# Performance work log

Hardware: AMD Instinct MI355X
Metric: run time of the kernel (lower is better)

Reference implementation:

```python
import jax, jax.numpy as jnp
import numpy as np

B, P = 16, 1024
D_TIME, NUM_MODS = 8, 22
DIM_S = NUM_MODS + D_TIME + 1  # 31
PHI_W, N_HEADS, DP = 32, 4, 32
PSI_W, PSI_L, RHO_W = 64, 64, 64
SQRT_DP = float(np.sqrt(DP))


def setup_inputs() -> dict:
    key = jax.random.key(0)
    ks = jax.random.split(key, 16)
    rn = lambda k, shape: jax.random.normal(k, shape, jnp.float32) * 0.05
    return dict(
        times=jax.random.uniform(ks[0], (B, P), jnp.float32) * 48.0,
        values=jax.random.normal(ks[1], (B, P), jnp.float32),
        measurements=jax.random.randint(ks[2], (B, P), 0, NUM_MODS + 1),
        non_pad_mask=jnp.ones((B, P, 1), jnp.float32),
        W_psi1=rn(ks[3], (DIM_S, PSI_W)), b_psi1=jnp.zeros((PSI_W,), jnp.float32),
        W_psi2=rn(ks[4], (PSI_W, PSI_L)), b_psi2=jnp.zeros((PSI_L,), jnp.float32),
        W_key=rn(ks[5], (DIM_S + PSI_L, N_HEADS * DP)), b_key=jnp.zeros((N_HEADS * DP,), jnp.float32),
        query=rn(ks[6], (N_HEADS, DP)),
        W_phi1=rn(ks[7], (DIM_S, PHI_W)), b_phi1=jnp.zeros((PHI_W,), jnp.float32),
        W_phi2=rn(ks[8], (PHI_W, PHI_W)), b_phi2=jnp.zeros((PHI_W,), jnp.float32),
        W_rho1=rn(ks[9], (N_HEADS * PHI_W, RHO_W)), b_rho1=jnp.zeros((RHO_W,), jnp.float32),
        W_rho2=rn(ks[10], (RHO_W, RHO_W)), b_rho2=jnp.zeros((RHO_W,), jnp.float32),
    )


def _temporal_enc(times):
    i = np.arange(D_TIME)
    pos_vec = jnp.asarray(10000.0 ** (2.0 * (i // 2) / D_TIME), jnp.float32)
    ang = times[:, :, None] / pos_vec  # [B,P,d_time]
    return jnp.where(jnp.asarray(i % 2 == 0), jnp.sin(ang), jnp.cos(ang))


def reference(times, values, measurements, non_pad_mask,
              W_psi1, b_psi1, W_psi2, b_psi2, W_key, b_key, query,
              W_phi1, b_phi1, W_phi2, b_phi2, W_rho1, b_rho1, W_rho2, b_rho2):
    m = non_pad_mask  # [B,P,1]
    te = _temporal_enc(times)
    oh = jax.nn.one_hot(measurements, NUM_MODS + 1, dtype=jnp.float32)[:, :, 1:]
    x = jnp.concatenate([te, values[:, :, None], oh], axis=-1)  # [B,P,dim_s]

    # CumulativeSetAttentionLayer: psi MLP -> cumulative mean -> keys . query
    psi = jax.nn.relu(jax.nn.relu(x @ W_psi1 + b_psi1) @ W_psi2 + b_psi2)  # [B,P,psi_l]
    cum = jnp.cumsum(psi * m, axis=1) / jnp.cumsum(m, axis=1)
    keys = (jnp.concatenate([x, cum], axis=-1) @ W_key + b_key).reshape(B, P, N_HEADS, DP)
    pre = jnp.einsum('bpmd,md->bpm', keys, query) / SQRT_DP  # [B,P,m]

    # phi MLP
    phi = jax.nn.relu(jax.nn.relu(x @ W_phi1 + b_phi1) @ W_phi2 + b_phi2) * m  # [B,P,phi_w]

    # cumulative softmax weighting (online path)
    cmax = jax.lax.cummax(pre, axis=1)  # [B,P,m], running max for stability
    D = jnp.exp(pre[:, None, :, :] - cmax[:, :, None, :])  # [B,P,Q,m]
    causal = jnp.arange(P)[:, None] >= jnp.arange(P)[None, :]  # keep Q <= P
    D = D * causal[None, :, :, None]
    E = D.sum(axis=2)  # [B,P,m]
    agg = jnp.einsum('bpqm,bqd->bpmd', D, phi) / E[:, :, :, None]
    agg = (agg * m[:, :, :, None]).reshape(B, P, N_HEADS * PHI_W)

    # rho MLP (return_sequences)
    out = jax.nn.relu(jax.nn.relu(agg @ W_rho1 + b_rho1) @ W_rho2 + b_rho2) * m
    return out
```

## Files before the change

kernel.cpp:

```cpp
#include <hip/hip_runtime.h>
#include <hip/hip_bf16.h>

#define B_ 16
#define P_ 1024
#define T_ (B_*P_)
#define CH_ 32
#define CL_ (P_/CH_)

constexpr int OFF_A     = 16;
constexpr int OFF_WPSI1 = 400;
constexpr int OFF_BPSI1 = OFF_WPSI1 + 1984;
constexpr int OFF_WPSI2 = OFF_BPSI1 + 64;
constexpr int OFF_BPSI2 = OFF_WPSI2 + 4096;
constexpr int OFF_WPHI1 = OFF_BPSI2 + 64;
constexpr int OFF_BPHI1 = OFF_WPHI1 + 992;
constexpr int OFF_WPHI2 = OFF_BPHI1 + 32;
constexpr int OFF_BPHI2 = OFF_WPHI2 + 1024;
constexpr int OFF_WRHO1 = OFF_BPHI2 + 32;
constexpr int OFF_BRHO1 = OFF_WRHO1 + 8192;
constexpr int OFF_WRHO2 = OFF_BRHO1 + 64;
constexpr int OFF_BRHO2 = OFF_WRHO2 + 4096;
constexpr int OFF_PHI   = OFF_BRHO2 + 64;
constexpr int OFF_Z     = OFF_PHI   + T_*32;
constexpr int OFF_PREX  = OFF_Z     + T_*4;
constexpr int OFF_EXPW  = OFF_PREX  + T_*4;
constexpr int OFF_CE    = OFF_EXPW  + T_*4;
constexpr int OFF_CS    = OFF_CE    + 2048;
constexpr int OFF_AGG   = OFF_CS    + 65536;

static __device__ __forceinline__ bool detect_f32(const void* mask_raw) {
  return ((*(const unsigned*)mask_raw) & 0xFFFFu) == 0u;
}
static __device__ __forceinline__ float ld_any(const void* src, int i, bool isf32) {
  if (isf32) return ((const float*)src)[i];
  return __bfloat162float(((const __hip_bfloat16*)src)[i]);
}

__global__ __launch_bounds__(256) void s01_prep(
    float* __restrict__ ws, const void* mask,
    const void* Wpsi1, const void* bpsi1, const void* Wpsi2, const void* bpsi2,
    const void* Wkey,  const void* bkey,  const void* query,
    const void* Wphi1, const void* bphi1, const void* Wphi2, const void* bphi2,
    const void* Wrho1, const void* brho1, const void* Wrho2, const void* brho2) {
  const bool isf32 = detect_f32(mask);
  if (blockIdx.x < 2) {
    const int gid = blockIdx.x * 256 + threadIdx.x;
    if (gid >= 384) return;
    const float inv_s = 0.17677669529663687f;
    const int h = gid & 3;
    const int j = gid >> 2;
    float s = 0.f;
    if (j < 95) {
      for (int d = 0; d < 32; ++d)
        s += ld_any(Wkey, j * 128 + h * 32 + d, isf32) * ld_any(query, h * 32 + d, isf32);
    } else {
      for (int d = 0; d < 32; ++d)
        s += ld_any(bkey, h * 32 + d, isf32) * ld_any(query, h * 32 + d, isf32);
    }
    ws[OFF_A + gid] = s * inv_s;
    return;
  }
  const int g  = (blockIdx.x - 2) * 256 + threadIdx.x;
  const int gs = (gridDim.x - 2) * 256;
  auto st = [&](int off, const void* src, int n) {
    for (int i = g; i < n; i += gs) ws[off + i] = ld_any(src, i, isf32);
  };
  st(OFF_WPSI1, Wpsi1, 1984); st(OFF_BPSI1, bpsi1, 64);
  st(OFF_WPSI2, Wpsi2, 4096); st(OFF_BPSI2, bpsi2, 64);
  st(OFF_WPHI1, Wphi1, 992);  st(OFF_BPHI1, bphi1, 32);
  st(OFF_WPHI2, Wphi2, 1024); st(OFF_BPHI2, bphi2, 32);
  st(OFF_WRHO1, Wrho1, 8192); st(OFF_BRHO1, brho1, 64);
  st(OFF_WRHO2, Wrho2, 4096); st(OFF_BRHO2, brho2, 64);
}

__global__ __launch_bounds__(256) void k1_token(float* __restrict__ ws,
                                                const int* __restrict__ measp,
                                                const void* __restrict__ times,
                                                const void* __restrict__ values,
                                                const void* __restrict__ mask) {
  __shared__ float sh1[4][64];
  __shared__ float sg1[4][32];
  const bool isf32 = detect_f32(mask);
  const int tid = threadIdx.x;
  const int wv  = __builtin_amdgcn_readfirstlane(tid >> 6);
  const int j   = tid & 63;
  const int t   = blockIdx.x * 4 + wv;

  const float tval = ld_any(times, t, isf32);
  const float vval = ld_any(values, t, isf32);
  const float mval = ld_any(mask, t, isf32);
  const int   meas = measp[t];
  const float sel  = (meas > 0) ? 1.f : 0.f;
  const int   mrow = (meas > 0) ? (8 + meas) : 0;

  float x[9];
  const float posv[4] = {1.f, 10.f, 100.f, 1000.f};
  #pragma unroll
  for (int k = 0; k < 4; ++k) {
    float s, c;
    __sincosf(tval / posv[k], &s, &c);
    x[2*k] = s; x[2*k+1] = c;
  }
  x[8] = vval;

  float h1 = ws[OFF_BPSI1 + j];
  #pragma unroll
  for (int i = 0; i < 9; ++i) h1 = fmaf(x[i], ws[OFF_WPSI1 + i * 64 + j], h1);
  h1 = fmaf(sel, ws[OFF_WPSI1 + mrow * 64 + j], h1);
  sh1[wv][j] = fmaxf(h1, 0.f);

  if (j < 32) {
    float g1 = ws[OFF_BPHI1 + j];
    #pragma unroll
    for (int i = 0; i < 9; ++i) g1 = fmaf(x[i], ws[OFF_WPHI1 + i * 32 + j], g1);
    g1 = fmaf(sel, ws[OFF_WPHI1 + mrow * 32 + j], g1);
    sg1[wv][j] = fmaxf(g1, 0.f);
  }
  __syncthreads();

  float h2 = ws[OFF_BPSI2 + j];
  #pragma unroll 8
  for (int i = 0; i < 64; ++i) h2 = fmaf(sh1[wv][i], ws[OFF_WPSI2 + i * 64 + j], h2);
  const float q = fmaxf(h2, 0.f) * mval;

  const float* a2 = ws + OFF_A + (31 + j) * 4;
  float z0 = q * a2[0], z1 = q * a2[1], z2 = q * a2[2], z3 = q * a2[3];
  #pragma unroll
  for (int off = 32; off; off >>= 1) {
    z0 += __shfl_xor(z0, off, 64);
    z1 += __shfl_xor(z1, off, 64);
    z2 += __shfl_xor(z2, off, 64);
    z3 += __shfl_xor(z3, off, 64);
  }
  if (j == 0) {
    float* zo = ws + OFF_Z + (size_t)t * 4;
    zo[0] = z0; zo[1] = z1; zo[2] = z2; zo[3] = z3;
  }

  if (j < 32) {
    float g2 = ws[OFF_BPHI2 + j];
    #pragma unroll 8
    for (int i = 0; i < 32; ++i) g2 = fmaf(sg1[wv][i], ws[OFF_WPHI2 + i * 32 + j], g2);
    ws[OFF_PHI + (size_t)t * 32 + j] = fmaxf(g2, 0.f) * mval;
  } else if (j < 36) {
    const int h = j - 32;
    float pr = ws[OFF_A + 380 + h];
    #pragma unroll
    for (int i = 0; i < 9; ++i) pr = fmaf(x[i], ws[OFF_A + i * 4 + h], pr);
    pr = fmaf(sel, ws[OFF_A + mrow * 4 + h], pr);
    ws[OFF_PREX + (size_t)t * 4 + h] = pr;
  }
}

__global__ __launch_bounds__(256) void k2_scanz(float* __restrict__ ws,
                                                const void* __restrict__ mask) {
  const int b   = blockIdx.x;
  const int tid = threadIdx.x;
  const bool isf32 = detect_f32(mask);
  __shared__ float sc[256], s0[256], s1[256], s2[256], s3[256];

  const float* zB = ws + OFF_Z + (size_t)b * P_ * 4;
  const int p0 = tid * 4;

  float lc[4], l0[4], l1[4], l2[4], l3[4];
  float c = 0.f, z0 = 0.f, z1 = 0.f, z2 = 0.f, z3 = 0.f;
  #pragma unroll
  for (int i = 0; i < 4; ++i) {
    c  += ld_any(mask, b * P_ + p0 + i, isf32);
    z0 += zB[(p0 + i) * 4 + 0]; z1 += zB[(p0 + i) * 4 + 1];
    z2 += zB[(p0 + i) * 4 + 2]; z3 += zB[(p0 + i) * 4 + 3];
    lc[i] = c; l0[i] = z0; l1[i] = z1; l2[i] = z2; l3[i] = z3;
  }

  float rc = c, r0 = z0, r1 = z1, r2 = z2, r3 = z3;
  sc[tid] = rc; s0[tid] = r0; s1[tid] = r1; s2[tid] = r2; s3[tid] = r3;
  __syncthreads();
  for (int off = 1; off < 256; off <<= 1) {
    float ac = 0.f, a0 = 0.f, a1 = 0.f, a2 = 0.f, a3 = 0.f;
    if (tid >= off) {
      ac = sc[tid - off]; a0 = s0[tid - off]; a1 = s1[tid - off];
      a2 = s2[tid - off]; a3 = s3[tid - off];
    }
    __syncthreads();
    rc += ac; r0 += a0; r1 += a1; r2 += a2; r3 += a3;
    sc[tid] = rc; s0[tid] = r0; s1[tid] = r1; s2[tid] = r2; s3[tid] = r3;
    __syncthreads();
  }
  const float ec = rc - c, e0 = r0 - z0, e1 = r1 - z1, e2 = r2 - z2, e3 = r3 - z3;

  const float* px = ws + OFF_PREX + (size_t)b * P_ * 4;
  float pre[4][4];
  float mx0 = -1e30f, mx1 = -1e30f, mx2 = -1e30f, mx3 = -1e30f;
  #pragma unroll
  for (int i = 0; i < 4; ++i) {
    const float inv = 1.f / (ec + lc[i]);
    const int p = p0 + i;
    pre[i][0] = px[p * 4 + 0] + (e0 + l0[i]) * inv;
    pre[i][1] = px[p * 4 + 1] + (e1 + l1[i]) * inv;
    pre[i][2] = px[p * 4 + 2] + (e2 + l2[i]) * inv;
    pre[i][3] = px[p * 4 + 3] + (e3 + l3[i]) * inv;
    mx0 = fmaxf(mx0, pre[i][0]); mx1 = fmaxf(mx1, pre[i][1]);
    mx2 = fmaxf(mx2, pre[i][2]); mx3 = fmaxf(mx3, pre[i][3]);
  }

  __syncthreads();
  s0[tid] = mx0; s1[tid] = mx1; s2[tid] = mx2; s3[tid] = mx3;
  __syncthreads();
  for (int off = 128; off; off >>= 1) {
    if (tid < off) {
      s0[tid] = fmaxf(s0[tid], s0[tid + off]);
      s1[tid] = fmaxf(s1[tid], s1[tid + off]);
      s2[tid] = fmaxf(s2[tid], s2[tid + off]);
      s3[tid] = fmaxf(s3[tid], s3[tid + off]);
    }
    __syncthreads();
  }
  const float M0 = s0[0], M1 = s1[0], M2 = s2[0], M3 = s3[0];

  float* eB = ws + OFF_EXPW + (size_t)b * P_ * 4;
  #pragma unroll
  for (int i = 0; i < 4; ++i) {
    const int p = p0 + i;
    eB[p * 4 + 0] = __expf(pre[i][0] - M0);
    eB[p * 4 + 1] = __expf(pre[i][1] - M1);
    eB[p * 4 + 2] = __expf(pre[i][2] - M2);
    eB[p * 4 + 3] = __expf(pre[i][3] - M3);
  }
}

__global__ __launch_bounds__(128) void k4a_sums(float* __restrict__ ws) {
  const int ch = blockIdx.x, b = blockIdx.y;
  const int h = threadIdx.x >> 5, d = threadIdx.x & 31;
  const float* eB   = ws + OFF_EXPW + (size_t)b * P_ * 4;
  const float* phiB = ws + OFF_PHI  + (size_t)b * P_ * 32;

  float E = 0.f, S = 0.f;
  const int pbeg = ch * CL_;
  #pragma unroll 4
  for (int p = pbeg; p < pbeg + CL_; ++p) {
    const float e  = eB[p * 4 + h];
    const float ph = phiB[p * 32 + d];
    E += e;
    S = fmaf(e, ph, S);
  }
  const int base = (b * CH_ + ch) * 4 + h;
  if (d == 0) ws[OFF_CE + base] = E;
  ws[OFF_CS + base * 32 + d] = S;
}

__global__ __launch_bounds__(128) void k4c_replay(float* __restrict__ ws,
                                                  const void* __restrict__ mask) {
  const int ch = blockIdx.x, b = blockIdx.y;
  const int h = threadIdx.x >> 5, d = threadIdx.x & 31;
  const bool isf32 = detect_f32(mask);
  const float* eB   = ws + OFF_EXPW + (size_t)b * P_ * 4;
  const float* phiB = ws + OFF_PHI  + (size_t)b * P_ * 32;
  float*       aggB = ws + OFF_AGG  + (size_t)b * P_ * 128;

  float E = 0.f, S = 0.f;
  for (int c2 = 0; c2 < ch; ++c2) {
    const int base2 = (b * CH_ + c2) * 4 + h;
    E += ws[OFF_CE + base2];
    S += ws[OFF_CS + base2 * 32 + d];
  }

  const int pbeg = ch * CL_;
  for (int p = pbeg; p < pbeg + CL_; ++p) {
    const float e  = eB[p * 4 + h];
    const float ph = phiB[p * 32 + d];
    E += e;
    S = fmaf(e, ph, S);
    aggB[p * 128 + h * 32 + d] = (S / E) * ld_any(mask, b * P_ + p, isf32);
  }
}

__global__ __launch_bounds__(256) void k5_rho(const float* __restrict__ ws,
                                              const void* __restrict__ mask_raw,
                                              void* __restrict__ out) {
  __shared__ float sW1[128 * 64];
  __shared__ float sH1[16][64];
  const int tid = threadIdx.x;
  for (int i = tid; i < 128 * 64; i += 256) sW1[i] = ws[OFF_WRHO1 + i];

  const int wv = __builtin_amdgcn_readfirstlane(tid >> 6);
  const int j  = tid & 63;
  const int t0 = blockIdx.x * 16 + wv * 4;
  const float* aggB = ws + OFF_AGG;

  const float b1 = ws[OFF_BRHO1 + j];
  float a0 = b1, a1 = b1, a2 = b1, a3 = b1;
  __syncthreads();

  #pragma unroll 8
  for (int i = 0; i < 128; ++i) {
    const float w = sW1[i * 64 + j];
    a0 = fmaf(aggB[(size_t)(t0 + 0) * 128 + i], w, a0);
    a1 = fmaf(aggB[(size_t)(t0 + 1) * 128 + i], w, a1);
    a2 = fmaf(aggB[(size_t)(t0 + 2) * 128 + i], w, a2);
    a3 = fmaf(aggB[(size_t)(t0 + 3) * 128 + i], w, a3);
  }
  sH1[wv * 4 + 0][j] = fmaxf(a0, 0.f);
  sH1[wv * 4 + 1][j] = fmaxf(a1, 0.f);
  sH1[wv * 4 + 2][j] = fmaxf(a2, 0.f);
  sH1[wv * 4 + 3][j] = fmaxf(a3, 0.f);
  __syncthreads();

  const float b2 = ws[OFF_BRHO2 + j];
  float o0 = b2, o1 = b2, o2 = b2, o3 = b2;
  #pragma unroll 8
  for (int i = 0; i < 64; ++i) {
    const float w = ws[OFF_WRHO2 + i * 64 + j];
    o0 = fmaf(sH1[wv * 4 + 0][i], w, o0);
    o1 = fmaf(sH1[wv * 4 + 1][i], w, o1);
    o2 = fmaf(sH1[wv * 4 + 2][i], w, o2);
    o3 = fmaf(sH1[wv * 4 + 3][i], w, o3);
  }

  const bool isf32 = detect_f32(mask_raw);
  float r[4] = {o0, o1, o2, o3};
  #pragma unroll
  for (int k = 0; k < 4; ++k) {
    const int t = t0 + k;
    const float v = fmaxf(r[k], 0.f) * ld_any(mask_raw, t, isf32);
    if (isf32) {
      ((float*)out)[(size_t)t * 64 + j] = v;
    } else {
      ((__hip_bfloat16*)out)[(size_t)t * 64 + j] = __float2bfloat16(v);
    }
  }
}

extern "C" void kernel_launch(void* const* d_in, const int* in_sizes, int n_in,
                              void* d_out, int out_size, void* d_ws, size_t ws_size,
                              hipStream_t stream) {
  const int* meas = (const int*)d_in[2];
  const void* times = d_in[0];
  const void* values = d_in[1];
  const void* mask = d_in[3];
  float* ws = (float*)d_ws;

  s01_prep<<<34, 256, 0, stream>>>(ws, mask,
                                   d_in[4], d_in[5], d_in[6], d_in[7],
                                   d_in[8], d_in[9], d_in[10],
                                   d_in[11], d_in[12], d_in[13], d_in[14],
                                   d_in[15], d_in[16], d_in[17], d_in[18]);
  k1_token<<<T_/4, 256, 0, stream>>>(ws, meas, times, values, mask);
  k2_scanz<<<B_, 256, 0, stream>>>(ws, mask);
  k4a_sums<<<dim3(CH_, B_), 128, 0, stream>>>(ws);
  k4c_replay<<<dim3(CH_, B_), 128, 0, stream>>>(ws, mask);
  k5_rho<<<T_/16, 256, 0, stream>>>(ws, mask, d_out);
}
```

Before: 160.3 us.

## Fuse all stages into one cooperative persistent kernel with grid syncs

Replaces the six separate kernel launches with a single cooperative kernel of 512 blocks that runs the weight prep, token MLPs, per-batch scan, chunk sums, replay and rho MLP as phases separated by grid.sync(). Shared memory is unioned across phases, and the token and rho stages loop over multiple tiles per block. This removes launch overhead and inter-kernel gaps. In exchange it adds grid-wide barrier costs and leaves most blocks idle during the 16-block scan phase.

```diff
diff --git a/kernel.cpp b/kernel.cpp
--- a/kernel.cpp
+++ b/kernel.cpp
@@ -1,11 +1,14 @@
 #include <hip/hip_runtime.h>
 #include <hip/hip_bf16.h>
+#include <hip/hip_cooperative_groups.h>
+namespace cg = cooperative_groups;
 
 #define B_ 16
 #define P_ 1024
 #define T_ (B_*P_)
 #define CH_ 32
 #define CL_ (P_/CH_)
+#define NBLK_ 512
 
 constexpr int OFF_A     = 16;
 constexpr int OFF_WPSI1 = 400;
@@ -36,317 +39,317 @@
   return __bfloat162float(((const __hip_bfloat16*)src)[i]);
 }
 
-__global__ __launch_bounds__(256) void s01_prep(
-    float* __restrict__ ws, const void* mask,
+__global__ __launch_bounds__(256, 2) void mega(
+    float* __restrict__ ws, const int* __restrict__ measp,
+    const void* times, const void* values, const void* mask, void* out,
     const void* Wpsi1, const void* bpsi1, const void* Wpsi2, const void* bpsi2,
     const void* Wkey,  const void* bkey,  const void* query,
     const void* Wphi1, const void* bphi1, const void* Wphi2, const void* bphi2,
     const void* Wrho1, const void* brho1, const void* Wrho2, const void* brho2) {
-  const bool isf32 = detect_f32(mask);
-  if (blockIdx.x < 2) {
-    const int gid = blockIdx.x * 256 + threadIdx.x;
-    if (gid >= 384) return;
-    const float inv_s = 0.17677669529663687f;
-    const int h = gid & 3;
-    const int j = gid >> 2;
-    float s = 0.f;
-    if (j < 95) {
-      for (int d = 0; d < 32; ++d)
-        s += ld_any(Wkey, j * 128 + h * 32 + d, isf32) * ld_any(query, h * 32 + d, isf32);
-    } else {
-      for (int d = 0; d < 32; ++d)
-        s += ld_any(bkey, h * 32 + d, isf32) * ld_any(query, h * 32 + d, isf32);
-    }
-    ws[OFF_A + gid] = s * inv_s;
-    return;
-  }
-  const int g  = (blockIdx.x - 2) * 256 + threadIdx.x;
-  const int gs = (gridDim.x - 2) * 256;
-  auto st = [&](int off, const void* src, int n) {
-    for (int i = g; i < n; i += gs) ws[off + i] = ld_any(src, i, isf32);
-  };
-  st(OFF_WPSI1, Wpsi1, 1984); st(OFF_BPSI1, bpsi1, 64);
-  st(OFF_WPSI2, Wpsi2, 4096); st(OFF_BPSI2, bpsi2, 64);
-  st(OFF_WPHI1, Wphi1, 992);  st(OFF_BPHI1, bphi1, 32);
-  st(OFF_WPHI2, Wphi2, 1024); st(OFF_BPHI2, bphi2, 32);
-  st(OFF_WRHO1, Wrho1, 8192); st(OFF_BRHO1, brho1, 64);
-  st(OFF_WRHO2, Wrho2, 4096); st(OFF_BRHO2, brho2, 64);
-}
-
-__global__ __launch_bounds__(256) void k1_token(float* __restrict__ ws,
-                                                const int* __restrict__ measp,
-                                                const void* __restrict__ times,
-                                                const void* __restrict__ values,
-                                                const void* __restrict__ mask) {
-  __shared__ float sh1[4][64];
-  __shared__ float sg1[4][32];
-  const bool isf32 = detect_f32(mask);
-  const int tid = threadIdx.x;
-  const int wv  = __builtin_amdgcn_readfirstlane(tid >> 6);
-  const int j   = tid & 63;
-  const int t   = blockIdx.x * 4 + wv;
-
-  const float tval = ld_any(times, t, isf32);
-  const float vval = ld_any(values, t, isf32);
-  const float mval = ld_any(mask, t, isf32);
-  const int   meas = measp[t];
-  const float sel  = (meas > 0) ? 1.f : 0.f;
-  const int   mrow = (meas > 0) ? (8 + meas) : 0;
-
-  float x[9];
-  const float posv[4] = {1.f, 10.f, 100.f, 1000.f};
-  #pragma unroll
-  for (int k = 0; k < 4; ++k) {
-    float s, c;
-    __sincosf(tval / posv[k], &s, &c);
-    x[2*k] = s; x[2*k+1] = c;
-  }
-  x[8] = vval;
-
-  float h1 = ws[OFF_BPSI1 + j];
-  #pragma unroll
-  for (int i = 0; i < 9; ++i) h1 = fmaf(x[i], ws[OFF_WPSI1 + i * 64 + j], h1);
-  h1 = fmaf(sel, ws[OFF_WPSI1 + mrow * 64 + j], h1);
-  sh1[wv][j] = fmaxf(h1, 0.f);
-
-  if (j < 32) {
-    float g1 = ws[OFF_BPHI1 + j];
-    #pragma unroll
-    for (int i = 0; i < 9; ++i) g1 = fmaf(x[i], ws[OFF_WPHI1 + i * 32 + j], g1);
-    g1 = fmaf(sel, ws[OFF_WPHI1 + mrow * 32 + j], g1);
-    sg1[wv][j] = fmaxf(g1, 0.f);
-  }
-  __syncthreads();
-
-  float h2 = ws[OFF_BPSI2 + j];
-  #pragma unroll 8
-  for (int i = 0; i < 64; ++i) h2 = fmaf(sh1[wv][i], ws[OFF_WPSI2 + i * 64 + j], h2);
-  const float q = fmaxf(h2, 0.f) * mval;
-
-  const float* a2 = ws + OFF_A + (31 + j) * 4;
-  float z0 = q * a2[0], z1 = q * a2[1], z2 = q * a2[2], z3 = q * a2[3];
-  #pragma unroll
-  for (int off = 32; off; off >>= 1) {
-    z0 += __shfl_xor(z0, off, 64);
-    z1 += __shfl_xor(z1, off, 64);
-    z2 += __shfl_xor(z2, off, 64);
-    z3 += __shfl_xor(z3, off, 64);
-  }
-  if (j == 0) {
-    float* zo = ws + OFF_Z + (size_t)t * 4;
-    zo[0] = z0; zo[1] = z1; zo[2] = z2; zo[3] = z3;
-  }
-
-  if (j < 32) {
-    float g2 = ws[OFF_BPHI2 + j];
-    #pragma unroll 8
-    for (int i = 0; i < 32; ++i) g2 = fmaf(sg1[wv][i], ws[OFF_WPHI2 + i * 32 + j], g2);
-    ws[OFF_PHI + (size_t)t * 32 + j] = fmaxf(g2, 0.f) * mval;
-  } else if (j < 36) {
-    const int h = j - 32;
-    float pr = ws[OFF_A + 380 + h];
-    #pragma unroll
-    for (int i = 0; i < 9; ++i) pr = fmaf(x[i], ws[OFF_A + i * 4 + h], pr);
-    pr = fmaf(sel, ws[OFF_A + mrow * 4 + h], pr);
-    ws[OFF_PREX + (size_t)t * 4 + h] = pr;
-  }
-}
-
-__global__ __launch_bounds__(256) void k2_scanz(float* __restrict__ ws,
-                                                const void* __restrict__ mask) {
-  const int b   = blockIdx.x;
+  cg::grid_group grid = cg::this_grid();
+  __shared__ union {
+    struct { float h1[4][64]; float g1[4][32]; } p1;
+    struct { float sc[256], s0[256], s1[256], s2[256], s3[256]; } p2;
+    struct { float w1[8192]; float h1[16][64]; } p5;
+  } sm;
+
   const int tid = threadIdx.x;
   const bool isf32 = detect_f32(mask);
-  __shared__ float sc[256], s0[256], s1[256], s2[256], s3[256];
-
-  const float* zB = ws + OFF_Z + (size_t)b * P_ * 4;
-  const int p0 = tid * 4;
-
-  float lc[4], l0[4], l1[4], l2[4], l3[4];
-  float c = 0.f, z0 = 0.f, z1 = 0.f, z2 = 0.f, z3 = 0.f;
-  #pragma unroll
-  for (int i = 0; i < 4; ++i) {
-    c  += ld_any(mask, b * P_ + p0 + i, isf32);
-    z0 += zB[(p0 + i) * 4 + 0]; z1 += zB[(p0 + i) * 4 + 1];
-    z2 += zB[(p0 + i) * 4 + 2]; z3 += zB[(p0 + i) * 4 + 3];
-    lc[i] = c; l0[i] = z0; l1[i] = z1; l2[i] = z2; l3[i] = z3;
-  }
-
-  float rc = c, r0 = z0, r1 = z1, r2 = z2, r3 = z3;
-  sc[tid] = rc; s0[tid] = r0; s1[tid] = r1; s2[tid] = r2; s3[tid] = r3;
-  __syncthreads();
-  for (int off = 1; off < 256; off <<= 1) {
-    float ac = 0.f, a0 = 0.f, a1 = 0.f, a2 = 0.f, a3 = 0.f;
-    if (tid >= off) {
-      ac = sc[tid - off]; a0 = s0[tid - off]; a1 = s1[tid - off];
-      a2 = s2[tid - off]; a3 = s3[tid - off];
-    }
-    __syncthreads();
-    rc += ac; r0 += a0; r1 += a1; r2 += a2; r3 += a3;
-    sc[tid] = rc; s0[tid] = r0; s1[tid] = r1; s2[tid] = r2; s3[tid] = r3;
-    __syncthreads();
-  }
-  const float ec = rc - c, e0 = r0 - z0, e1 = r1 - z1, e2 = r2 - z2, e3 = r3 - z3;
-
-  const float* px = ws + OFF_PREX + (size_t)b * P_ * 4;
-  float pre[4][4];
-  float mx0 = -1e30f, mx1 = -1e30f, mx2 = -1e30f, mx3 = -1e30f;
-  #pragma unroll
-  for (int i = 0; i < 4; ++i) {
-    const float inv = 1.f / (ec + lc[i]);
-    const int p = p0 + i;
-    pre[i][0] = px[p * 4 + 0] + (e0 + l0[i]) * inv;
-    pre[i][1] = px[p * 4 + 1] + (e1 + l1[i]) * inv;
-    pre[i][2] = px[p * 4 + 2] + (e2 + l2[i]) * inv;
-    pre[i][3] = px[p * 4 + 3] + (e3 + l3[i]) * inv;
-    mx0 = fmaxf(mx0, pre[i][0]); mx1 = fmaxf(mx1, pre[i][1]);
-    mx2 = fmaxf(mx2, pre[i][2]); mx3 = fmaxf(mx3, pre[i][3]);
-  }
-
-  __syncthreads();
-  s0[tid] = mx0; s1[tid] = mx1; s2[tid] = mx2; s3[tid] = mx3;
-  __syncthreads();
-  for (int off = 128; off; off >>= 1) {
-    if (tid < off) {
-      s0[tid] = fmaxf(s0[tid], s0[tid + off]);
-      s1[tid] = fmaxf(s1[tid], s1[tid + off]);
-      s2[tid] = fmaxf(s2[tid], s2[tid + off]);
-      s3[tid] = fmaxf(s3[tid], s3[tid + off]);
-    }
-    __syncthreads();
-  }
-  const float M0 = s0[0], M1 = s1[0], M2 = s2[0], M3 = s3[0];
-
-  float* eB = ws + OFF_EXPW + (size_t)b * P_ * 4;
-  #pragma unroll
-  for (int i = 0; i < 4; ++i) {
-    const int p = p0 + i;
-    eB[p * 4 + 0] = __expf(pre[i][0] - M0);
-    eB[p * 4 + 1] = __expf(pre[i][1] - M1);
-    eB[p * 4 + 2] = __expf(pre[i][2] - M2);
-    eB[p * 4 + 3] = __expf(pre[i][3] - M3);
-  }
-}
-
-__global__ __launch_bounds__(128) void k4a_sums(float* __restrict__ ws) {
-  const int ch = blockIdx.x, b = blockIdx.y;
-  const int h = threadIdx.x >> 5, d = threadIdx.x & 31;
-  const float* eB   = ws + OFF_EXPW + (size_t)b * P_ * 4;
-  const float* phiB = ws + OFF_PHI  + (size_t)b * P_ * 32;
-
-  float E = 0.f, S = 0.f;
-  const int pbeg = ch * CL_;
-  #pragma unroll 4
-  for (int p = pbeg; p < pbeg + CL_; ++p) {
-    const float e  = eB[p * 4 + h];
-    const float ph = phiB[p * 32 + d];
-    E += e;
-    S = fmaf(e, ph, S);
-  }
-  const int base = (b * CH_ + ch) * 4 + h;
-  if (d == 0) ws[OFF_CE + base] = E;
-  ws[OFF_CS + base * 32 + d] = S;
-}
-
-__global__ __launch_bounds__(128) void k4c_replay(float* __restrict__ ws,
-                                                  const void* __restrict__ mask) {
-  const int ch = blockIdx.x, b = blockIdx.y;
-  const int h = threadIdx.x >> 5, d = threadIdx.x & 31;
-  const bool isf32 = detect_f32(mask);
-  const float* eB   = ws + OFF_EXPW + (size_t)b * P_ * 4;
-  const float* phiB = ws + OFF_PHI  + (size_t)b * P_ * 32;
-  float*       aggB = ws + OFF_AGG  + (size_t)b * P_ * 128;
-
-  float E = 0.f, S = 0.f;
-  for (int c2 = 0; c2 < ch; ++c2) {
-    const int base2 = (b * CH_ + c2) * 4 + h;
-    E += ws[OFF_CE + base2];
-    S += ws[OFF_CS + base2 * 32 + d];
-  }
-
-  const int pbeg = ch * CL_;
-  for (int p = pbeg; p < pbeg + CL_; ++p) {
-    const float e  = eB[p * 4 + h];
-    const float ph = phiB[p * 32 + d];
-    E += e;
-    S = fmaf(e, ph, S);
-    aggB[p * 128 + h * 32 + d] = (S / E) * ld_any(mask, b * P_ + p, isf32);
-  }
-}
-
-__global__ __launch_bounds__(256) void k5_rho(const float* __restrict__ ws,
-                                              const void* __restrict__ mask_raw,
-                                              void* __restrict__ out) {
-  __shared__ float sW1[128 * 64];
-  __shared__ float sH1[16][64];
-  const int tid = threadIdx.x;
-  for (int i = tid; i < 128 * 64; i += 256) sW1[i] = ws[OFF_WRHO1 + i];
-
   const int wv = __builtin_amdgcn_readfirstlane(tid >> 6);
   const int j  = tid & 63;
-  const int t0 = blockIdx.x * 16 + wv * 4;
+
+  {
+    const int g  = blockIdx.x * 256 + tid;
+    if (g < 384) {
+      const float inv_s = 0.17677669529663687f;
+      const int h = g & 3;
+      const int jj = g >> 2;
+      float s = 0.f;
+      if (jj < 95) {
+        for (int d = 0; d < 32; ++d)
+          s += ld_any(Wkey, jj * 128 + h * 32 + d, isf32) * ld_any(query, h * 32 + d, isf32);
+      } else {
+        for (int d = 0; d < 32; ++d)
+          s += ld_any(bkey, h * 32 + d, isf32) * ld_any(query, h * 32 + d, isf32);
+      }
+      ws[OFF_A + g] = s * inv_s;
+    }
+    const int gs = NBLK_ * 256;
+    auto st = [&](int off, const void* src, int n) {
+      for (int i = g; i < n; i += gs) ws[off + i] = ld_any(src, i, isf32);
+    };
+    st(OFF_WPSI1, Wpsi1, 1984); st(OFF_BPSI1, bpsi1, 64);
+    st(OFF_WPSI2, Wpsi2, 4096); st(OFF_BPSI2, bpsi2, 64);
+    st(OFF_WPHI1, Wphi1, 992);  st(OFF_BPHI1, bphi1, 32);
+    st(OFF_WPHI2, Wphi2, 1024); st(OFF_BPHI2, bphi2, 32);
+    st(OFF_WRHO1, Wrho1, 8192); st(OFF_BRHO1, brho1, 64);
+    st(OFF_WRHO2, Wrho2, 4096); st(OFF_BRHO2, brho2, 64);
+  }
+  grid.sync();
+
+  for (int it = 0; it < 8; ++it) {
+    const int t = it * (NBLK_ * 4) + blockIdx.x * 4 + wv;
+
+    const float tval = ld_any(times, t, isf32);
+    const float vval = ld_any(values, t, isf32);
+    const float mval = ld_any(mask, t, isf32);
+    const int   meas = measp[t];
+    const float sel  = (meas > 0) ? 1.f : 0.f;
+    const int   mrow = (meas > 0) ? (8 + meas) : 0;
+
+    float x[9];
+    const float posv[4] = {1.f, 10.f, 100.f, 1000.f};
+    #pragma unroll
+    for (int k = 0; k < 4; ++k) {
+      float s, c;
+      __sincosf(tval / posv[k], &s, &c);
+      x[2*k] = s; x[2*k+1] = c;
+    }
+    x[8] = vval;
+
+    float h1 = ws[OFF_BPSI1 + j];
+    #pragma unroll
+    for (int i = 0; i < 9; ++i) h1 = fmaf(x[i], ws[OFF_WPSI1 + i * 64 + j], h1);
+    h1 = fmaf(sel, ws[OFF_WPSI1 + mrow * 64 + j], h1);
+    sm.p1.h1[wv][j] = fmaxf(h1, 0.f);
+
+    if (j < 32) {
+      float g1 = ws[OFF_BPHI1 + j];
+      #pragma unroll
+      for (int i = 0; i < 9; ++i) g1 = fmaf(x[i], ws[OFF_WPHI1 + i * 32 + j], g1);
+      g1 = fmaf(sel, ws[OFF_WPHI1 + mrow * 32 + j], g1);
+      sm.p1.g1[wv][j] = fmaxf(g1, 0.f);
+    }
+    __syncthreads();
+
+    float h2 = ws[OFF_BPSI2 + j];
+    #pragma unroll 8
+    for (int i = 0; i < 64; ++i) h2 = fmaf(sm.p1.h1[wv][i], ws[OFF_WPSI2 + i * 64 + j], h2);
+    const float q = fmaxf(h2, 0.f) * mval;
+
+    const float* a2 = ws + OFF_A + (31 + j) * 4;
+    float z0 = q * a2[0], z1 = q * a2[1], z2 = q * a2[2], z3 = q * a2[3];
+    #pragma unroll
+    for (int off = 32; off; off >>= 1) {
+      z0 += __shfl_xor(z0, off, 64);
+      z1 += __shfl_xor(z1, off, 64);
+      z2 += __shfl_xor(z2, off, 64);
+      z3 += __shfl_xor(z3, off, 64);
+    }
+    if (j == 0) {
+      float* zo = ws + OFF_Z + (size_t)t * 4;
+      zo[0] = z0; zo[1] = z1; zo[2] = z2; zo[3] = z3;
+    }
+
+    if (j < 32) {
+      float g2 = ws[OFF_BPHI2 + j];
+      #pragma unroll 8
+      for (int i = 0; i < 32; ++i) g2 = fmaf(sm.p1.g1[wv][i], ws[OFF_WPHI2 + i * 32 + j], g2);
+      ws[OFF_PHI + (size_t)t * 32 + j] = fmaxf(g2, 0.f) * mval;
+    } else if (j < 36) {
+      const int h = j - 32;
+      float pr = ws[OFF_A + 380 + h];
+      #pragma unroll
+      for (int i = 0; i < 9; ++i) pr = fmaf(x[i], ws[OFF_A + i * 4 + h], pr);
+      pr = fmaf(sel, ws[OFF_A + mrow * 4 + h], pr);
+      ws[OFF_PREX + (size_t)t * 4 + h] = pr;
+    }
+    __syncthreads();
+  }
+  grid.sync();
+
+  if (blockIdx.x < B_) {
+    const int b = blockIdx.x;
+    float* sc = sm.p2.sc; float* s0 = sm.p2.s0; float* s1 = sm.p2.s1;
+    float* s2 = sm.p2.s2; float* s3 = sm.p2.s3;
+
+    const float* zB = ws + OFF_Z + (size_t)b * P_ * 4;
+    const int p0 = tid * 4;
+
+    float lc[4], l0[4], l1[4], l2[4], l3[4];
+    float c = 0.f, z0 = 0.f, z1 = 0.f, z2 = 0.f, z3 = 0.f;
+    #pragma unroll
+    for (int i = 0; i < 4; ++i) {
+      c  += ld_any(mask, b * P_ + p0 + i, isf32);
+      z0 += zB[(p0 + i) * 4 + 0]; z1 += zB[(p0 + i) * 4 + 1];
+      z2 += zB[(p0 + i) * 4 + 2]; z3 += zB[(p0 + i) * 4 + 3];
+      lc[i] = c; l0[i] = z0; l1[i] = z1; l2[i] = z2; l3[i] = z3;
+    }
+
+    float rc = c, r0 = z0, r1 = z1, r2 = z2, r3 = z3;
+    sc[tid] = rc; s0[tid] = r0; s1[tid] = r1; s2[tid] = r2; s3[tid] = r3;
+    __syncthreads();
+    for (int off = 1; off < 256; off <<= 1) {
+      float ac = 0.f, a0 = 0.f, a1 = 0.f, a2 = 0.f, a3 = 0.f;
+      if (tid >= off) {
+        ac = sc[tid - off]; a0 = s0[tid - off]; a1 = s1[tid - off];
+        a2 = s2[tid - off]; a3 = s3[tid - off];
+      }
+      __syncthreads();
+      rc += ac; r0 += a0; r1 += a1; r2 += a2; r3 += a3;
+      sc[tid] = rc; s0[tid] = r0; s1[tid] = r1; s2[tid] = r2; s3[tid] = r3;
+      __syncthreads();
+    }
+    const float ec = rc - c, e0 = r0 - z0, e1 = r1 - z1, e2 = r2 - z2, e3 = r3 - z3;
+
+    const float* px = ws + OFF_PREX + (size_t)b * P_ * 4;
+    float pre[4][4];
+    float mx0 = -1e30f, mx1 = -1e30f, mx2 = -1e30f, mx3 = -1e30f;
+    #pragma unroll
+    for (int i = 0; i < 4; ++i) {
+      const float inv = 1.f / (ec + lc[i]);
+      const int p = p0 + i;
+      pre[i][0] = px[p * 4 + 0] + (e0 + l0[i]) * inv;
+      pre[i][1] = px[p * 4 + 1] + (e1 + l1[i]) * inv;
+      pre[i][2] = px[p * 4 + 2] + (e2 + l2[i]) * inv;
+      pre[i][3] = px[p * 4 + 3] + (e3 + l3[i]) * inv;
+      mx0 = fmaxf(mx0, pre[i][0]); mx1 = fmaxf(mx1, pre[i][1]);
+      mx2 = fmaxf(mx2, pre[i][2]); mx3 = fmaxf(mx3, pre[i][3]);
+    }
+
+    __syncthreads();
+    s0[tid] = mx0; s1[tid] = mx1; s2[tid] = mx2; s3[tid] = mx3;
+    __syncthreads();
+    for (int off = 128; off; off >>= 1) {
+      if (tid < off) {
+        s0[tid] = fmaxf(s0[tid], s0[tid + off]);
+        s1[tid] = fmaxf(s1[tid], s1[tid + off]);
+        s2[tid] = fmaxf(s2[tid], s2[tid + off]);
+        s3[tid] = fmaxf(s3[tid], s3[tid + off]);
+      }
+      __syncthreads();
+    }
+    const float M0 = s0[0], M1 = s1[0], M2 = s2[0], M3 = s3[0];
+
+    float* eB = ws + OFF_EXPW + (size_t)b * P_ * 4;
+    #pragma unroll
+    for (int i = 0; i < 4; ++i) {
+      const int p = p0 + i;
+      eB[p * 4 + 0] = __expf(pre[i][0] - M0);
+      eB[p * 4 + 1] = __expf(pre[i][1] - M1);
+      eB[p * 4 + 2] = __expf(pre[i][2] - M2);
+      eB[p * 4 + 3] = __expf(pre[i][3] - M3);
+    }
+  }
+  grid.sync();
+
+  if (tid < 128) {
+    const int ch = blockIdx.x & 31, b = blockIdx.x >> 5;
+    const int h = tid >> 5, d = tid & 31;
+    const float* eB   = ws + OFF_EXPW + (size_t)b * P_ * 4;
+    const float* phiB = ws + OFF_PHI  + (size_t)b * P_ * 32;
+
+    float E = 0.f, S = 0.f;
+    const int pbeg = ch * CL_;
+    #pragma unroll 4
+    for (int p = pbeg; p < pbeg + CL_; ++p) {
+      const float e  = eB[p * 4 + h];
+      const float ph = phiB[p * 32 + d];
+      E += e;
+      S = fmaf(e, ph, S);
+    }
+    const int base = (b * CH_ + ch) * 4 + h;
+    if (d == 0) ws[OFF_CE + base] = E;
+    ws[OFF_CS + base * 32 + d] = S;
+  }
+  grid.sync();
+
+  if (tid < 128) {
+    const int ch = blockIdx.x & 31, b = blockIdx.x >> 5;
+    const int h = tid >> 5, d = tid & 31;
+    const float* eB   = ws + OFF_EXPW + (size_t)b * P_ * 4;
+    const float* phiB = ws + OFF_PHI  + (size_t)b * P_ * 32;
+    float*       aggB = ws + OFF_AGG  + (size_t)b * P_ * 128;
+
+    float E = 0.f, S = 0.f;
+    for (int c2 = 0; c2 < ch; ++c2) {
+      const int base2 = (b * CH_ + c2) * 4 + h;
+      E += ws[OFF_CE + base2];
+      S += ws[OFF_CS + base2 * 32 + d];
+    }
+    const int pbeg = ch * CL_;
+    for (int p = pbeg; p < pbeg + CL_; ++p) {
+      const float e  = eB[p * 4 + h];
+      const float ph = phiB[p * 32 + d];
+      E += e;
+      S = fmaf(e, ph, S);
+      aggB[p * 128 + h * 32 + d] = (S / E) * ld_any(mask, b * P_ + p, isf32);
+    }
+  }
+  grid.sync();
+
+  for (int i = tid; i < 8192; i += 256) sm.p5.w1[i] = ws[OFF_WRHO1 + i];
+  const float b1 = ws[OFF_BRHO1 + j];
+  const float b2 = ws[OFF_BRHO2 + j];
+  __syncthreads();
+
   const float* aggB = ws + OFF_AGG;
-
-  const float b1 = ws[OFF_BRHO1 + j];
-  float a0 = b1, a1 = b1, a2 = b1, a3 = b1;
-  __syncthreads();
-
-  #pragma unroll 8
-  for (int i = 0; i < 128; ++i) {
-    const float w = sW1[i * 64 + j];
-    a0 = fmaf(aggB[(size_t)(t0 + 0) * 128 + i], w, a0);
-    a1 = fmaf(aggB[(size_t)(t0 + 1) * 128 + i], w, a1);
-    a2 = fmaf(aggB[(size_t)(t0 + 2) * 128 + i], w, a2);
-    a3 = fmaf(aggB[(size_t)(t0 + 3) * 128 + i], w, a3);
-  }
-  sH1[wv * 4 + 0][j] = fmaxf(a0, 0.f);
-  sH1[wv * 4 + 1][j] = fmaxf(a1, 0.f);
-  sH1[wv * 4 + 2][j] = fmaxf(a2, 0.f);
-  sH1[wv * 4 + 3][j] = fmaxf(a3, 0.f);
-  __syncthreads();
-
-  const float b2 = ws[OFF_BRHO2 + j];
-  float o0 = b2, o1 = b2, o2 = b2, o3 = b2;
-  #pragma unroll 8
-  for (int i = 0; i < 64; ++i) {
-    const float w = ws[OFF_WRHO2 + i * 64 + j];
-    o0 = fmaf(sH1[wv * 4 + 0][i], w, o0);
-    o1 = fmaf(sH1[wv * 4 + 1][i], w, o1);
-    o2 = fmaf(sH1[wv * 4 + 2][i], w, o2);
-    o3 = fmaf(sH1[wv * 4 + 3][i], w, o3);
-  }
-
-  const bool isf32 = detect_f32(mask_raw);
-  float r[4] = {o0, o1, o2, o3};
-  #pragma unroll
-  for (int k = 0; k < 4; ++k) {
-    const int t = t0 + k;
-    const float v = fmaxf(r[k], 0.f) * ld_any(mask_raw, t, isf32);
-    if (isf32) {
-      ((float*)out)[(size_t)t * 64 + j] = v;
-    } else {
-      ((__hip_bfloat16*)out)[(size_t)t * 64 + j] = __float2bfloat16(v);
-    }
+  for (int it = 0; it < 2; ++it) {
+    const int t0 = (blockIdx.x * 2 + it) * 16 + wv * 4;
+
+    float a0 = b1, a1 = b1, a2 = b1, a3 = b1;
+    #pragma unroll 8
+    for (int i = 0; i < 128; ++i) {
+      const float w = sm.p5.w1[i * 64 + j];
+      a0 = fmaf(aggB[(size_t)(t0 + 0) * 128 + i], w, a0);
+      a1 = fmaf(aggB[(size_t)(t0 + 1) * 128 + i], w, a1);
+      a2 = fmaf(aggB[(size_t)(t0 + 2) * 128 + i], w, a2);
+      a3 = fmaf(aggB[(size_t)(t0 + 3) * 128 + i], w, a3);
+    }
+    sm.p5.h1[wv * 4 + 0][j] = fmaxf(a0, 0.f);
+    sm.p5.h1[wv * 4 + 1][j] = fmaxf(a1, 0.f);
+    sm.p5.h1[wv * 4 + 2][j] = fmaxf(a2, 0.f);
+    sm.p5.h1[wv * 4 + 3][j] = fmaxf(a3, 0.f);
+    __syncthreads();
+
+    float o0 = b2, o1 = b2, o2 = b2, o3 = b2;
+    #pragma unroll 8
+    for (int i = 0; i < 64; ++i) {
+      const float w = ws[OFF_WRHO2 + i * 64 + j];
+      o0 = fmaf(sm.p5.h1[wv * 4 + 0][i], w, o0);
+      o1 = fmaf(sm.p5.h1[wv * 4 + 1][i], w, o1);
+      o2 = fmaf(sm.p5.h1[wv * 4 + 2][i], w, o2);
+      o3 = fmaf(sm.p5.h1[wv * 4 + 3][i], w, o3);
+    }
+
+    const float r[4] = {o0, o1, o2, o3};
+    #pragma unroll
+    for (int k = 0; k < 4; ++k) {
+      const int t = t0 + k;
+      const float v = fmaxf(r[k], 0.f) * ld_any(mask, t, isf32);
+      if (isf32) {
+        ((float*)out)[(size_t)t * 64 + j] = v;
+      } else {
+        ((__hip_bfloat16*)out)[(size_t)t * 64 + j] = __float2bfloat16(v);
+      }
+    }
+    __syncthreads();
   }
 }
 
 extern "C" void kernel_launch(void* const* d_in, const int* in_sizes, int n_in,
                               void* d_out, int out_size, void* d_ws, size_t ws_size,
                               hipStream_t stream) {
+  float* ws = (float*)d_ws;
   const int* meas = (const int*)d_in[2];
-  const void* times = d_in[0];
+  const void* times  = d_in[0];
   const void* values = d_in[1];
-  const void* mask = d_in[3];
-  float* ws = (float*)d_ws;
-
-  s01_prep<<<34, 256, 0, stream>>>(ws, mask,
-                                   d_in[4], d_in[5], d_in[6], d_in[7],
-                                   d_in[8], d_in[9], d_in[10],
-                                   d_in[11], d_in[12], d_in[13], d_in[14],
-                                   d_in[15], d_in[16], d_in[17], d_in[18]);
-  k1_token<<<T_/4, 256, 0, stream>>>(ws, meas, times, values, mask);
-  k2_scanz<<<B_, 256, 0, stream>>>(ws, mask);
-  k4a_sums<<<dim3(CH_, B_), 128, 0, stream>>>(ws);
-  k4c_replay<<<dim3(CH_, B_), 128, 0, stream>>>(ws, mask);
-  k5_rho<<<T_/16, 256, 0, stream>>>(ws, mask, d_out);
+  const void* mask   = d_in[3];
+  void* out = d_out;
+  const void* Wpsi1 = d_in[4];  const void* bpsi1 = d_in[5];
+  const void* Wpsi2 = d_in[6];  const void* bpsi2 = d_in[7];
+  const void* Wkey  = d_in[8];  const void* bkey  = d_in[9];
+  const void* query = d_in[10];
+  const void* Wphi1 = d_in[11]; const void* bphi1 = d_in[12];
+  const void* Wphi2 = d_in[13]; const void* bphi2 = d_in[14];
+  const void* Wrho1 = d_in[15]; const void* brho1 = d_in[16];
+  const void* Wrho2 = d_in[17]; const void* brho2 = d_in[18];
+
+  void* args[] = {&ws, &meas, &times, &values, &mask, &out,
+                  &Wpsi1, &bpsi1, &Wpsi2, &bpsi2,
+                  &Wkey, &bkey, &query,
+                  &Wphi1, &bphi1, &Wphi2, &bphi2,
+                  &Wrho1, &brho1, &Wrho2, &brho2};
+  hipLaunchCooperativeKernel((const void*)mega, dim3(NBLK_), dim3(256),
+                             args, 0, stream);
 }
```

New measurement: 469.8 us. 193% more time.

## Fuse chunk-sum and replay kernels by recomputing prefix sums per block

Applied to the files above, without the earlier changes.

Drops the separate chunk-sum kernel and its scratch buffers. Each block now recomputes the running exp-weight and weighted-phi prefix over all earlier positions directly, using four independent accumulators to expose more parallelism. This removes one kernel launch and the global round-trip for the chunk totals. In exchange, later chunks do quadratically more redundant work (up to a full sequence scan), and floating-point summation order changes.

```diff
diff --git a/kernel.cpp b/kernel.cpp
--- a/kernel.cpp
+++ b/kernel.cpp
@@ -24,9 +24,7 @@
 constexpr int OFF_Z     = OFF_PHI   + T_*32;
 constexpr int OFF_PREX  = OFF_Z     + T_*4;
 constexpr int OFF_EXPW  = OFF_PREX  + T_*4;
-constexpr int OFF_CE    = OFF_EXPW  + T_*4;
-constexpr int OFF_CS    = OFF_CE    + 2048;
-constexpr int OFF_AGG   = OFF_CS    + 65536;
+constexpr int OFF_AGG   = OFF_EXPW  + T_*4;
 
 static __device__ __forceinline__ bool detect_f32(const void* mask_raw) {
   return ((*(const unsigned*)mask_raw) & 0xFFFFu) == 0u;
@@ -228,28 +226,8 @@
   }
 }
 
-__global__ __launch_bounds__(128) void k4a_sums(float* __restrict__ ws) {
-  const int ch = blockIdx.x, b = blockIdx.y;
-  const int h = threadIdx.x >> 5, d = threadIdx.x & 31;
-  const float* eB   = ws + OFF_EXPW + (size_t)b * P_ * 4;
-  const float* phiB = ws + OFF_PHI  + (size_t)b * P_ * 32;
-
-  float E = 0.f, S = 0.f;
-  const int pbeg = ch * CL_;
-  #pragma unroll 4
-  for (int p = pbeg; p < pbeg + CL_; ++p) {
-    const float e  = eB[p * 4 + h];
-    const float ph = phiB[p * 32 + d];
-    E += e;
-    S = fmaf(e, ph, S);
-  }
-  const int base = (b * CH_ + ch) * 4 + h;
-  if (d == 0) ws[OFF_CE + base] = E;
-  ws[OFF_CS + base * 32 + d] = S;
-}
-
-__global__ __launch_bounds__(128) void k4c_replay(float* __restrict__ ws,
-                                                  const void* __restrict__ mask) {
+__global__ __launch_bounds__(128) void k4_fused(float* __restrict__ ws,
+                                                const void* __restrict__ mask) {
   const int ch = blockIdx.x, b = blockIdx.y;
   const int h = threadIdx.x >> 5, d = threadIdx.x & 31;
   const bool isf32 = detect_f32(mask);
@@ -257,14 +235,24 @@
   const float* phiB = ws + OFF_PHI  + (size_t)b * P_ * 32;
   float*       aggB = ws + OFF_AGG  + (size_t)b * P_ * 128;
 
-  float E = 0.f, S = 0.f;
-  for (int c2 = 0; c2 < ch; ++c2) {
-    const int base2 = (b * CH_ + c2) * 4 + h;
-    E += ws[OFF_CE + base2];
-    S += ws[OFF_CS + base2 * 32 + d];
-  }
-
   const int pbeg = ch * CL_;
+
+  float E0 = 0.f, E1 = 0.f, E2 = 0.f, E3 = 0.f;
+  float S0 = 0.f, S1 = 0.f, S2 = 0.f, S3 = 0.f;
+  for (int p = 0; p < pbeg; p += 4) {
+    const float ea = eB[(p + 0) * 4 + h];
+    const float eb = eB[(p + 1) * 4 + h];
+    const float ec = eB[(p + 2) * 4 + h];
+    const float ed = eB[(p + 3) * 4 + h];
+    E0 += ea; E1 += eb; E2 += ec; E3 += ed;
+    S0 = fmaf(ea, phiB[(p + 0) * 32 + d], S0);
+    S1 = fmaf(eb, phiB[(p + 1) * 32 + d], S1);
+    S2 = fmaf(ec, phiB[(p + 2) * 32 + d], S2);
+    S3 = fmaf(ed, phiB[(p + 3) * 32 + d], S3);
+  }
+  float E = (E0 + E1) + (E2 + E3);
+  float S = (S0 + S1) + (S2 + S3);
+
   for (int p = pbeg; p < pbeg + CL_; ++p) {
     const float e  = eB[p * 4 + h];
     const float ph = phiB[p * 32 + d];
@@ -346,7 +334,6 @@
                                    d_in[15], d_in[16], d_in[17], d_in[18]);
   k1_token<<<T_/4, 256, 0, stream>>>(ws, meas, times, values, mask);
   k2_scanz<<<B_, 256, 0, stream>>>(ws, mask);
-  k4a_sums<<<dim3(CH_, B_), 128, 0, stream>>>(ws);
-  k4c_replay<<<dim3(CH_, B_), 128, 0, stream>>>(ws, mask);
+  k4_fused<<<dim3(CH_, B_), 128, 0, stream>>>(ws, mask);
   k5_rho<<<T_/16, 256, 0, stream>>>(ws, mask, d_out);
 }
```

Result: slower. 226.0 us (+41.0%).

## Fold weight prep into token and rho kernels, removing the prep launch

Applied to the files above, without the earlier changes.

Removes the separate prep kernel that copied weights into the workspace and precomputed the key-query fold. The token kernel now computes the 384-entry key·query projection per block into shared memory and reads MLP weights directly from the inputs. The rho kernel likewise loads its weights straight from the inputs. This saves a launch and a workspace round trip, but adds redundant per-block fold computation and dtype-converting loads in hot loops.

```diff
diff --git a/kernel.cpp b/kernel.cpp
--- a/kernel.cpp
+++ b/kernel.cpp
@@ -7,20 +7,7 @@
 #define CH_ 32
 #define CL_ (P_/CH_)
 
-constexpr int OFF_A     = 16;
-constexpr int OFF_WPSI1 = 400;
-constexpr int OFF_BPSI1 = OFF_WPSI1 + 1984;
-constexpr int OFF_WPSI2 = OFF_BPSI1 + 64;
-constexpr int OFF_BPSI2 = OFF_WPSI2 + 4096;
-constexpr int OFF_WPHI1 = OFF_BPSI2 + 64;
-constexpr int OFF_BPHI1 = OFF_WPHI1 + 992;
-constexpr int OFF_WPHI2 = OFF_BPHI1 + 32;
-constexpr int OFF_BPHI2 = OFF_WPHI2 + 1024;
-constexpr int OFF_WRHO1 = OFF_BPHI2 + 32;
-constexpr int OFF_BRHO1 = OFF_WRHO1 + 8192;
-constexpr int OFF_WRHO2 = OFF_BRHO1 + 64;
-constexpr int OFF_BRHO2 = OFF_WRHO2 + 4096;
-constexpr int OFF_PHI   = OFF_BRHO2 + 64;
+constexpr int OFF_PHI   = 16;
 constexpr int OFF_Z     = OFF_PHI   + T_*32;
 constexpr int OFF_PREX  = OFF_Z     + T_*4;
 constexpr int OFF_EXPW  = OFF_PREX  + T_*4;
@@ -36,52 +23,37 @@
   return __bfloat162float(((const __hip_bfloat16*)src)[i]);
 }
 
-__global__ __launch_bounds__(256) void s01_prep(
-    float* __restrict__ ws, const void* mask,
-    const void* Wpsi1, const void* bpsi1, const void* Wpsi2, const void* bpsi2,
-    const void* Wkey,  const void* bkey,  const void* query,
-    const void* Wphi1, const void* bphi1, const void* Wphi2, const void* bphi2,
-    const void* Wrho1, const void* brho1, const void* Wrho2, const void* brho2) {
+__global__ __launch_bounds__(256) void k1_token(
+    float* __restrict__ ws, const int* __restrict__ measp,
+    const void* __restrict__ times, const void* __restrict__ values,
+    const void* __restrict__ mask,
+    const void* __restrict__ Wpsi1, const void* __restrict__ bpsi1,
+    const void* __restrict__ Wpsi2, const void* __restrict__ bpsi2,
+    const void* __restrict__ Wkey,  const void* __restrict__ bkey,
+    const void* __restrict__ query,
+    const void* __restrict__ Wphi1, const void* __restrict__ bphi1,
+    const void* __restrict__ Wphi2, const void* __restrict__ bphi2) {
+  __shared__ float sA[384];
+  __shared__ float sh1[4][64];
+  __shared__ float sg1[4][32];
   const bool isf32 = detect_f32(mask);
-  if (blockIdx.x < 2) {
-    const int gid = blockIdx.x * 256 + threadIdx.x;
-    if (gid >= 384) return;
+  const int tid = threadIdx.x;
+
+  for (int gid = tid; gid < 384; gid += 256) {
     const float inv_s = 0.17677669529663687f;
     const int h = gid & 3;
-    const int j = gid >> 2;
+    const int jj = gid >> 2;
     float s = 0.f;
-    if (j < 95) {
+    if (jj < 95) {
       for (int d = 0; d < 32; ++d)
-        s += ld_any(Wkey, j * 128 + h * 32 + d, isf32) * ld_any(query, h * 32 + d, isf32);
+        s += ld_any(Wkey, jj * 128 + h * 32 + d, isf32) * ld_any(query, h * 32 + d, isf32);
     } else {
       for (int d = 0; d < 32; ++d)
         s += ld_any(bkey, h * 32 + d, isf32) * ld_any(query, h * 32 + d, isf32);
     }
-    ws[OFF_A + gid] = s * inv_s;
-    return;
-  }
-  const int g  = (blockIdx.x - 2) * 256 + threadIdx.x;
-  const int gs = (gridDim.x - 2) * 256;
-  auto st = [&](int off, const void* src, int n) {
-    for (int i = g; i < n; i += gs) ws[off + i] = ld_any(src, i, isf32);
-  };
-  st(OFF_WPSI1, Wpsi1, 1984); st(OFF_BPSI1, bpsi1, 64);
-  st(OFF_WPSI2, Wpsi2, 4096); st(OFF_BPSI2, bpsi2, 64);
-  st(OFF_WPHI1, Wphi1, 992);  st(OFF_BPHI1, bphi1, 32);
-  st(OFF_WPHI2, Wphi2, 1024); st(OFF_BPHI2, bphi2, 32);
-  st(OFF_WRHO1, Wrho1, 8192); st(OFF_BRHO1, brho1, 64);
-  st(OFF_WRHO2, Wrho2, 4096); st(OFF_BRHO2, brho2, 64);
-}
-
-__global__ __launch_bounds__(256) void k1_token(float* __restrict__ ws,
-                                                const int* __restrict__ measp,
-                                                const void* __restrict__ times,
-                                                const void* __restrict__ values,
-                                                const void* __restrict__ mask) {
-  __shared__ float sh1[4][64];
-  __shared__ float sg1[4][32];
-  const bool isf32 = detect_f32(mask);
-  const int tid = threadIdx.x;
+    sA[gid] = s * inv_s;
+  }
+
   const int wv  = __builtin_amdgcn_readfirstlane(tid >> 6);
   const int j   = tid & 63;
   const int t   = blockIdx.x * 4 + wv;
@@ -103,27 +75,27 @@
   }
   x[8] = vval;
 
-  float h1 = ws[OFF_BPSI1 + j];
-  #pragma unroll
-  for (int i = 0; i < 9; ++i) h1 = fmaf(x[i], ws[OFF_WPSI1 + i * 64 + j], h1);
-  h1 = fmaf(sel, ws[OFF_WPSI1 + mrow * 64 + j], h1);
+  float h1 = ld_any(bpsi1, j, isf32);
+  #pragma unroll
+  for (int i = 0; i < 9; ++i) h1 = fmaf(x[i], ld_any(Wpsi1, i * 64 + j, isf32), h1);
+  h1 = fmaf(sel, ld_any(Wpsi1, mrow * 64 + j, isf32), h1);
   sh1[wv][j] = fmaxf(h1, 0.f);
 
   if (j < 32) {
-    float g1 = ws[OFF_BPHI1 + j];
+    float g1 = ld_any(bphi1, j, isf32);
     #pragma unroll
-    for (int i = 0; i < 9; ++i) g1 = fmaf(x[i], ws[OFF_WPHI1 + i * 32 + j], g1);
-    g1 = fmaf(sel, ws[OFF_WPHI1 + mrow * 32 + j], g1);
+    for (int i = 0; i < 9; ++i) g1 = fmaf(x[i], ld_any(Wphi1, i * 32 + j, isf32), g1);
+    g1 = fmaf(sel, ld_any(Wphi1, mrow * 32 + j, isf32), g1);
     sg1[wv][j] = fmaxf(g1, 0.f);
   }
   __syncthreads();
 
-  float h2 = ws[OFF_BPSI2 + j];
+  float h2 = ld_any(bpsi2, j, isf32);
   #pragma unroll 8
-  for (int i = 0; i < 64; ++i) h2 = fmaf(sh1[wv][i], ws[OFF_WPSI2 + i * 64 + j], h2);
+  for (int i = 0; i < 64; ++i) h2 = fmaf(sh1[wv][i], ld_any(Wpsi2, i * 64 + j, isf32), h2);
   const float q = fmaxf(h2, 0.f) * mval;
 
-  const float* a2 = ws + OFF_A + (31 + j) * 4;
+  const float* a2 = sA + (31 + j) * 4;
   float z0 = q * a2[0], z1 = q * a2[1], z2 = q * a2[2], z3 = q * a2[3];
   #pragma unroll
   for (int off = 32; off; off >>= 1) {
@@ -138,16 +110,16 @@
   }
 
   if (j < 32) {
-    float g2 = ws[OFF_BPHI2 + j];
+    float g2 = ld_any(bphi2, j, isf32);
     #pragma unroll 8
-    for (int i = 0; i < 32; ++i) g2 = fmaf(sg1[wv][i], ws[OFF_WPHI2 + i * 32 + j], g2);
+    for (int i = 0; i < 32; ++i) g2 = fmaf(sg1[wv][i], ld_any(Wphi2, i * 32 + j, isf32), g2);
     ws[OFF_PHI + (size_t)t * 32 + j] = fmaxf(g2, 0.f) * mval;
   } else if (j < 36) {
     const int h = j - 32;
-    float pr = ws[OFF_A + 380 + h];
+    float pr = sA[380 + h];
     #pragma unroll
-    for (int i = 0; i < 9; ++i) pr = fmaf(x[i], ws[OFF_A + i * 4 + h], pr);
-    pr = fmaf(sel, ws[OFF_A + mrow * 4 + h], pr);
+    for (int i = 0; i < 9; ++i) pr = fmaf(x[i], sA[i * 4 + h], pr);
+    pr = fmaf(sel, sA[mrow * 4 + h], pr);
     ws[OFF_PREX + (size_t)t * 4 + h] = pr;
   }
 }
@@ -274,20 +246,23 @@
   }
 }
 
-__global__ __launch_bounds__(256) void k5_rho(const float* __restrict__ ws,
-                                              const void* __restrict__ mask_raw,
-                                              void* __restrict__ out) {
+__global__ __launch_bounds__(256) void k5_rho(
+    const float* __restrict__ ws, const void* __restrict__ mask_raw,
+    const void* __restrict__ Wrho1, const void* __restrict__ brho1,
+    const void* __restrict__ Wrho2, const void* __restrict__ brho2,
+    void* __restrict__ out) {
   __shared__ float sW1[128 * 64];
   __shared__ float sH1[16][64];
   const int tid = threadIdx.x;
-  for (int i = tid; i < 128 * 64; i += 256) sW1[i] = ws[OFF_WRHO1 + i];
+  const bool isf32 = detect_f32(mask_raw);
+  for (int i = tid; i < 128 * 64; i += 256) sW1[i] = ld_any(Wrho1, i, isf32);
 
   const int wv = __builtin_amdgcn_readfirstlane(tid >> 6);
   const int j  = tid & 63;
   const int t0 = blockIdx.x * 16 + wv * 4;
   const float* aggB = ws + OFF_AGG;
 
-  const float b1 = ws[OFF_BRHO1 + j];
+  const float b1 = ld_any(brho1, j, isf32);
   float a0 = b1, a1 = b1, a2 = b1, a3 = b1;
   __syncthreads();
 
@@ -305,18 +280,17 @@
   sH1[wv * 4 + 3][j] = fmaxf(a3, 0.f);
   __syncthreads();
 
-  const float b2 = ws[OFF_BRHO2 + j];
+  const float b2 = ld_any(brho2, j, isf32);
   float o0 = b2, o1 = b2, o2 = b2, o3 = b2;
   #pragma unroll 8
   for (int i = 0; i < 64; ++i) {
-    const float w = ws[OFF_WRHO2 + i * 64 + j];
+    const float w = ld_any(Wrho2, i * 64 + j, isf32);
     o0 = fmaf(sH1[wv * 4 + 0][i], w, o0);
     o1 = fmaf(sH1[wv * 4 + 1][i], w, o1);
     o2 = fmaf(sH1[wv * 4 + 2][i], w, o2);
     o3 = fmaf(sH1[wv * 4 + 3][i], w, o3);
   }
 
-  const bool isf32 = detect_f32(mask_raw);
   float r[4] = {o0, o1, o2, o3};
   #pragma unroll
   for (int k = 0; k < 4; ++k) {
@@ -339,14 +313,13 @@
   const void* mask = d_in[3];
   float* ws = (float*)d_ws;
 
-  s01_prep<<<34, 256, 0, stream>>>(ws, mask,
-                                   d_in[4], d_in[5], d_in[6], d_in[7],
-                                   d_in[8], d_in[9], d_in[10],
-                                   d_in[11], d_in[12], d_in[13], d_in[14],
-                                   d_in[15], d_in[16], d_in[17], d_in[18]);
-  k1_token<<<T_/4, 256, 0, stream>>>(ws, meas, times, values, mask);
+  k1_token<<<T_/4, 256, 0, stream>>>(ws, meas, times, values, mask,
+                                     d_in[4], d_in[5], d_in[6], d_in[7],
+                                     d_in[8], d_in[9], d_in[10],
+                                     d_in[11], d_in[12], d_in[13], d_in[14]);
   k2_scanz<<<B_, 256, 0, stream>>>(ws, mask);
   k4a_sums<<<dim3(CH_, B_), 128, 0, stream>>>(ws);
   k4c_replay<<<dim3(CH_, B_), 128, 0, stream>>>(ws, mask);
-  k5_rho<<<T_/16, 256, 0, stream>>>(ws, mask, d_out);
-}
+  k5_rho<<<T_/16, 256, 0, stream>>>(ws, mask,
+                                    d_in[15], d_in[16], d_in[17], d_in[18], d_out);
+}
```

New measurement: 272.7 us. +70.1%, slower.
